# Optimization experiments

Measured on AMD Instinct MI355X. Metric: run time of the kernel, lower is better.

Reference implementation:

```python
import jax, jax.numpy as jnp
import numpy as np
from jax import lax

B, T, H, IN = 1024, 100, 512, 4  # batch, seq len (fixed 100 in source), hidden, nucleotide dim


def _lstm_cell(x, h, c, Wih, Whh, b):
    # PyTorch gate order: i, f, g, o ; b = b_ih + b_hh
    gates = x @ Wih.T + h @ Whh.T + b
    i, f, g, o = jnp.split(gates, 4, axis=-1)
    c = jax.nn.sigmoid(f) * c + jax.nn.sigmoid(i) * jnp.tanh(g)
    h = jax.nn.sigmoid(o) * jnp.tanh(c)
    return h, c


def _run_layer(xs, Wih, Whh, b):
    # xs: [T, B, in] -> ys: [T, B, H], final (h, c)
    Bn = xs.shape[1]
    h0 = jnp.zeros((Bn, H), xs.dtype)
    c0 = jnp.zeros((Bn, H), xs.dtype)

    def step(carry, x):
        h, c = carry
        h, c = _lstm_cell(x, h, c, Wih, Whh, b)
        return (h, c), h

    (h, c), ys = lax.scan(step, (h0, c0), xs)
    return ys, h, c


def setup_inputs() -> dict:
    key = jax.random.key(0)
    ks = jax.random.split(key, 16)
    s = lambda fan: 1.0 / np.sqrt(fan)

    def W(k, shape, fan):
        return jax.random.uniform(k, shape, jnp.float32, -s(fan), s(fan))

    inp = {
        "X": jax.random.normal(ks[0], (B, T, IN), jnp.float32),
        "epoch": 10,
        # encoder LSTM (2 layers)
        "enc_Wih0": W(ks[1], (4 * H, IN), H),
        "enc_Whh0": W(ks[2], (4 * H, H), H),
        "enc_b0": jnp.zeros((4 * H,), jnp.float32),
        "enc_Wih1": W(ks[3], (4 * H, H), H),
        "enc_Whh1": W(ks[4], (4 * H, H), H),
        "enc_b1": jnp.zeros((4 * H,), jnp.float32),
        # decoder LSTM (2 layers, input dim = seq_in_dim = 4)
        "dec_Wih0": W(ks[5], (4 * H, IN), H),
        "dec_Whh0": W(ks[6], (4 * H, H), H),
        "dec_b0": jnp.zeros((4 * H,), jnp.float32),
        "dec_Wih1": W(ks[7], (4 * H, H), H),
        "dec_Whh1": W(ks[8], (4 * H, H), H),
        "dec_b1": jnp.zeros((4 * H,), jnp.float32),
        # predict_MLP = Linear(H, 4)
        "Wp": W(ks[9], (IN, H), H),
        "bp": jnp.zeros((IN,), jnp.float32),
    }
    return inp


def reference(X, epoch, enc_Wih0, enc_Whh0, enc_b0, enc_Wih1, enc_Whh1, enc_b1,
              dec_Wih0, dec_Whh0, dec_b0, dec_Wih1, dec_Whh1, dec_b1, Wp, bp):
    # ---- Encoder: 2-layer LSTM over X (batch_first -> scan over time) ----
    xs = jnp.swapaxes(X, 0, 1)  # [T, B, 4]
    ys0, h0e, c0e = _run_layer(xs, enc_Wih0, enc_Whh0, enc_b0)
    _, h1e, c1e = _run_layer(ys0, enc_Wih1, enc_Whh1, enc_b1)

    #      discretize_input=False) ----
    Bn = X.shape[0]
    x_init = jnp.zeros((Bn, IN), X.dtype)

    def dec_step(carry, _):
        x, h0, c0, h1, c1 = carry
        h0, c0 = _lstm_cell(x, h0, c0, dec_Wih0, dec_Whh0, dec_b0)
        h1, c1 = _lstm_cell(h0, h1, c1, dec_Wih1, dec_Whh1, dec_b1)
        pred = h1 @ Wp.T + bp                 # [B, 4] logits
        x_next = jax.nn.softmax(pred, axis=-1)
        return (x_next, h0, c0, h1, c1), pred

    _, preds = lax.scan(dec_step, (x_init, h0e, c0e, h1e, c1e), None, length=T)
    # out_seq list of [B,1,4] in torch -> stacked [B, 100, 4]
    return jnp.swapaxes(preds, 0, 1)
```

## Files before the change

### kernel.cpp

```cpp
#include <hip/hip_runtime.h>
#include <math.h>
#include <stdint.h>

typedef _Float16 f16;
typedef _Float16 f16x8 __attribute__((ext_vector_type(8)));
typedef float f32x4 __attribute__((ext_vector_type(4)));

#define BATCH 1024
#define HD    512
#define TST   100
#define BUFSZ 49152

__device__ __forceinline__ float4 coh_ld_x4(const void* p) {
    float4 v;
    asm volatile("global_load_dwordx4 %0, %1, off sc0 sc1" : "=v"(v) : "v"(p) : "memory");
    return v;
}
__device__ __forceinline__ float4 ld_x4(const void* p) {
    float4 v;
    asm volatile("global_load_dwordx4 %0, %1, off" : "=v"(v) : "v"(p) : "memory");
    return v;
}
__device__ __forceinline__ void coh_store_u32(uint32_t* p, uint32_t v) {
    asm volatile("global_store_dword %0, %1, off sc0 sc1" :: "v"(p), "v"(v) : "memory");
}
__device__ __forceinline__ void coh_store_i32(int* p, int v) {
    asm volatile("global_store_dword %0, %1, off sc0 sc1" :: "v"(p), "v"(v) : "memory");
}
__device__ __forceinline__ int coh_load_i32(const int* p) {
    int v;
    asm volatile("global_load_dword %0, %1, off sc0 sc1\n\ts_waitcnt vmcnt(0)"
                 : "=v"(v) : "v"(p) : "memory");
    return v;
}
__device__ __forceinline__ void drain_vm() {
    asm volatile("s_waitcnt vmcnt(0)" ::: "memory");
    __builtin_amdgcn_sched_barrier(0);
}

__global__ void split_w(const float* __restrict__ src0, int ksplit,
                        const float* __restrict__ src1, int NKT, f16* __restrict__ out)
{
    int c = blockIdx.x * 256 + threadIdx.x;
    int total = 16 * NKT * 2048;
    if (c >= total) return;
    int u = c & 2047;
    int t2 = c >> 11;
    int kt = t2 % NKT;
    int mt = t2 / NKT;
    int line = u >> 4;
    int s = (u & 15) ^ (line & 15);
    int plane = s >> 3, o = s & 7;
    int m = mt * 128 + line;
    int row = (m & 3) * HD + (m >> 2);
    int kb = kt * 64 + o * 8;
    f16 v[8];
    #pragma unroll
    for (int e = 0; e < 8; ++e) {
        int k = kb + e;
        float w = (k < ksplit) ? src0[(size_t)row * ksplit + k]
                               : src1[(size_t)row * HD + (k - ksplit)];
        float w32 = w * 32.0f;
        f16 hi = (f16)w32;
        v[e] = plane ? (f16)((w32 - (float)hi) * 2048.0f) : hi;
    }
    *(f16x8*)(out + (size_t)c * 8) = *(f16x8*)v;
}

__global__ void prep_b4(const float* __restrict__ b, float* __restrict__ bt) {
    int c = blockIdx.x * 256 + threadIdx.x;
    if (c < 2048) bt[c] = b[(c & 3) * HD + (c >> 2)];
}

__global__ void prep_wih4(const float* __restrict__ W, float* __restrict__ o) {
    int c = blockIdx.x * 256 + threadIdx.x;
    if (c < 8192) {
        int j = c & 3, g = (c >> 2) & 3, hl = c >> 4;
        o[c] = W[(size_t)(g * HD + hl) * 4 + j];
    }
}

__device__ __forceinline__ void publish(int* cell, int epoch) {
    drain_vm();
    __syncthreads();
    if (threadIdx.x == 0)
        coh_store_i32(cell, epoch);
}

__device__ __forceinline__ void wait2(const int* a, int ta, const int* b, int tb) {
    if (threadIdx.x < 64) {
        const int l = threadIdx.x & 15;
        const bool useB = (threadIdx.x & 16) != 0;
        const int* p = (useB ? b : a) + l * 16;
        const int tgt = useB ? tb : ta;
        for (;;) {
            int v = coh_load_i32(p);
            if (__all(v >= tgt)) break;
            __builtin_amdgcn_s_sleep(2);
        }
    }
    __syncthreads();
}

template<int NKT, bool RANK4>
__device__ __forceinline__ void layer_step(
    const f16* __restrict__ Wst, const f16* __restrict__ src1, const f16* __restrict__ src2,
    const float* __restrict__ wih4, const float* __restrict__ xin, int xstride,
    const float* __restrict__ bt4, float* __restrict__ cT, f16* __restrict__ hout,
    char* smem, int mt, int nt)
{
    const int tid = threadIdx.x;
    const int lane = tid & 63;
    const int wv = tid >> 6;
    const int wm = wv & 1, wn = wv >> 1;
    const int l15 = lane & 15, j = lane >> 4;
    const int n0 = nt * 64;

    const int q = (j ^ l15) << 4;
    int ALr[4], BLb[2];
    #pragma unroll
    for (int f = 0; f < 4; ++f) ALr[f] = (wm * 64 + f * 16 + l15) * 256;
    #pragma unroll
    for (int fn = 0; fn < 2; ++fn) BLb[fn] = 32768 + (wn * 32 + fn * 16 + l15) * 256;

    float4 ra[8], rb0[4], rb1[4], xv[2];

    auto issueA = [&](int kt) {
        const f16* ga = Wst + ((size_t)mt * NKT + kt) * 2048 * 8;
        #pragma unroll
        for (int i = 0; i < 8; ++i)
            ra[i] = ld_x4(ga + (size_t)(i * 256 + tid) * 8);
    };
    auto issueB = [&](int kt, float4 (&rb)[4]) {
        #pragma unroll
        for (int i = 0; i < 4; ++i) {
            int v = i * 256 + tid;
            int line = v >> 4;
            int s = (v & 15) ^ (line & 15);
            int ks = kt * 64 + (s & 7) * 8;
            const f16* sp = src1; int kl = ks;
            if (NKT == 16 && ks >= 512) { sp = src2; kl = ks - 512; }
            rb[i] = coh_ld_x4(sp + (size_t)(n0 + line) * 1024 + (s >> 3) * 512 + kl);
        }
    };

    f32x4 accA[4][2] = {};
    f32x4 accB[4][2] = {};

    auto step = [&](int kt, float4 (&rb)[4], bool last) {
        char* buf = smem + (kt & 1) * BUFSZ;
        if (last) asm volatile("s_waitcnt vmcnt(0)" ::: "memory");
        else      asm volatile("s_waitcnt vmcnt(4)" ::: "memory");
        __builtin_amdgcn_sched_barrier(0);
        #pragma unroll
        for (int i = 0; i < 8; ++i) *(float4*)(buf + (i * 256 + tid) * 16) = ra[i];
        #pragma unroll
        for (int i = 0; i < 4; ++i) *(float4*)(buf + 32768 + (i * 256 + tid) * 16) = rb[i];
        if (kt + 1 < NKT) issueA(kt + 1);
        if (kt + 2 < NKT) issueB(kt + 2, rb);
        __syncthreads();
        #pragma unroll
        for (int i = 0; i < 2; ++i) {
            const int off = (i << 6) ^ q;
            f16x8 ah[4], al[4], bh[2], bl[2];
            #pragma unroll
            for (int f = 0; f < 4; ++f) {
                ah[f] = *(const f16x8*)(buf + ALr[f] + off);
                al[f] = *(const f16x8*)(buf + ALr[f] + (off ^ 0x80));
            }
            #pragma unroll
            for (int fn = 0; fn < 2; ++fn) {
                bh[fn] = *(const f16x8*)(buf + BLb[fn] + off);
                bl[fn] = *(const f16x8*)(buf + BLb[fn] + (off ^ 0x80));
            }
            #pragma unroll
            for (int f = 0; f < 4; ++f)
                #pragma unroll
                for (int fn = 0; fn < 2; ++fn) {
                    accA[f][fn] = __builtin_amdgcn_mfma_f32_16x16x32_f16(ah[f], bh[fn], accA[f][fn], 0, 0, 0);
                    accB[f][fn] = __builtin_amdgcn_mfma_f32_16x16x32_f16(al[f], bh[fn], accB[f][fn], 0, 0, 0);
                    accB[f][fn] = __builtin_amdgcn_mfma_f32_16x16x32_f16(ah[f], bl[fn], accB[f][fn], 0, 0, 0);
                }
        }
    };

    if (RANK4) {
        #pragma unroll
        for (int fn = 0; fn < 2; ++fn) {
            const int n = n0 + wn * 32 + fn * 16 + l15;
            xv[fn] = coh_ld_x4(xin + (size_t)n * xstride);
        }
    }
    issueB(0, rb0);
    issueA(0);
    issueB(1, rb1);

    for (int kt = 0; kt < NKT; kt += 2) {
        step(kt,     rb0, false);
        step(kt + 1, rb1, kt + 2 == NKT);
    }

    const float sA = 1.0f / 1024.0f;
    const float sB = 1.0f / (1024.0f * 2048.0f);

    uint32_t* htile = (uint32_t*)smem;
    #pragma unroll
    for (int f = 0; f < 4; ++f) {
        const int hl_loc = wm * 16 + f * 4 + j;
        const int hl = mt * 32 + hl_loc;
        const float4 bv = *(const float4*)(bt4 + hl * 4);
        #pragma unroll
        for (int fn = 0; fn < 2; ++fn) {
            const int n_loc = wn * 32 + fn * 16 + l15;
            const int n = n0 + n_loc;
            float g0 = accA[f][fn][0] * sA + accB[f][fn][0] * sB + bv.x;
            float g1 = accA[f][fn][1] * sA + accB[f][fn][1] * sB + bv.y;
            float g2 = accA[f][fn][2] * sA + accB[f][fn][2] * sB + bv.z;
            float g3 = accA[f][fn][3] * sA + accB[f][fn][3] * sB + bv.w;
            if (RANK4) {
                const float4* wr = (const float4*)(wih4 + hl * 16);
                const float4 x4 = xv[fn];
                g0 += wr[0].x * x4.x + wr[0].y * x4.y + wr[0].z * x4.z + wr[0].w * x4.w;
                g1 += wr[1].x * x4.x + wr[1].y * x4.y + wr[1].z * x4.z + wr[1].w * x4.w;
                g2 += wr[2].x * x4.x + wr[2].y * x4.y + wr[2].z * x4.z + wr[2].w * x4.w;
                g3 += wr[3].x * x4.x + wr[3].y * x4.y + wr[3].z * x4.z + wr[3].w * x4.w;
            }
            const size_t co = (size_t)hl * 1024 + n;
            const float cold = cT[co];
            const float si = 1.0f / (1.0f + expf(-g0));
            const float sf = 1.0f / (1.0f + expf(-g1));
            const float so = 1.0f / (1.0f + expf(-g3));
            const float cn = sf * cold + si * tanhf(g2);
            const float hn = so * tanhf(cn);
            cT[co] = cn;
            const float h32 = hn * 32.0f;
            const f16 hi = (f16)h32;
            const f16 lo = (f16)((h32 - (float)hi) * 2048.0f);
            uint32_t pk = ((uint32_t)__builtin_bit_cast(uint16_t, lo) << 16)
                        | (uint32_t)__builtin_bit_cast(uint16_t, hi);
            htile[n_loc * 33 + hl_loc] = pk;
        }
    }
    __syncthreads();
    uint32_t* h32out = (uint32_t*)hout;
    #pragma unroll
    for (int i = 0; i < 8; ++i) {
        int u = i * 256 + tid;
        int n_loc = u >> 5;
        int r = u & 31;
        int plane = r >> 4;
        int p = r & 15;
        uint32_t t0 = htile[n_loc * 33 + 2 * p];
        uint32_t t1 = htile[n_loc * 33 + 2 * p + 1];
        uint32_t w = plane ? ((t1 & 0xffff0000u) | (t0 >> 16))
                           : ((t1 << 16) | (t0 & 0xffffu));
        coh_store_u32(h32out + (size_t)(n0 + n_loc) * 512 + plane * 256 + mt * 16 + p, w);
    }
}

__device__ __forceinline__ void pred_step(
    const f16* __restrict__ h1, const float* __restrict__ Wp, const float* __restrict__ bp,
    float* __restrict__ outp, float* __restrict__ xfb, int t, int mt, int nt)
{
    const int lane = threadIdx.x & 63;
    const int wv = threadIdx.x >> 6;
    const int n = nt * 64 + mt * 4 + wv;
    const f16* hr = h1 + (size_t)n * 1024;
    const int k0 = lane * 8;
    float4 hv4 = coh_ld_x4(hr + k0);
    float4 lv4 = coh_ld_x4(hr + 512 + k0);
    drain_vm();
    f16x8 hv = __builtin_bit_cast(f16x8, hv4);
    f16x8 lv = __builtin_bit_cast(f16x8, lv4);
    float h[8];
    #pragma unroll
    for (int e = 0; e < 8; ++e)
        h[e] = (float)hv[e] * 0.03125f + (float)lv[e] * (1.0f / 65536.0f);
    float a[4] = {};
    #pragma unroll
    for (int g = 0; g < 4; ++g) {
        const float4 wa = *(const float4*)(Wp + g * HD + k0);
        const float4 wb = *(const float4*)(Wp + g * HD + k0 + 4);
        a[g] = h[0]*wa.x + h[1]*wa.y + h[2]*wa.z + h[3]*wa.w
             + h[4]*wb.x + h[5]*wb.y + h[6]*wb.z + h[7]*wb.w;
    }
    #pragma unroll
    for (int off = 32; off > 0; off >>= 1) {
        a[0] += __shfl_xor(a[0], off);
        a[1] += __shfl_xor(a[1], off);
        a[2] += __shfl_xor(a[2], off);
        a[3] += __shfl_xor(a[3], off);
    }
    if (lane == 0) {
        const float4 bv = *(const float4*)bp;
        float v0 = a[0] + bv.x, v1 = a[1] + bv.y, v2 = a[2] + bv.z, v3 = a[3] + bv.w;
        float* op = outp + (size_t)n * (TST * 4) + t * 4;
        op[0] = v0; op[1] = v1; op[2] = v2; op[3] = v3;
        float m = fmaxf(fmaxf(v0, v1), fmaxf(v2, v3));
        float e0 = expf(v0 - m), e1 = expf(v1 - m), e2 = expf(v2 - m), e3 = expf(v3 - m);
        float inv = 1.0f / (e0 + e1 + e2 + e3);
        uint32_t* xp = (uint32_t*)(xfb + n * 4);
        float s0 = e0 * inv, s1 = e1 * inv, s2 = e2 * inv, s3 = e3 * inv;
        coh_store_u32(xp + 0, __builtin_bit_cast(uint32_t, s0));
        coh_store_u32(xp + 1, __builtin_bit_cast(uint32_t, s1));
        coh_store_u32(xp + 2, __builtin_bit_cast(uint32_t, s2));
        coh_store_u32(xp + 3, __builtin_bit_cast(uint32_t, s3));
    }
}

struct Params {
    const f16 *WE0, *WE1, *WD0, *WD1;
    const float *wih4E, *wih4D, *btE0, *btE1, *btD0, *btD1;
    const float *X, *Wp, *bp;
    f16 *h0a, *h0b, *h1a, *h1b;
    float *c0, *c1;
    float *xfb0, *xfb1;
    float *out;
    int *f0, *f1, *fp;
};

__launch_bounds__(256, 1) __global__ void lstm_persistent(Params P)
{
    __shared__ __align__(16) char smem[2 * BUFSZ];
    const int bx = blockIdx.x;
    const int mt = ((bx & 7) << 1) | ((bx >> 3) & 1);
    const int nt = bx >> 4;
    int* f0g = P.f0 + nt * 256;
    int* f1g = P.f1 + nt * 256;
    int* fpg = P.fp + nt * 256;
    int* my0 = f0g + mt * 16;
    int* my1 = f1g + mt * 16;
    int* myp = fpg + mt * 16;
    f16* h0b_[2] = { P.h0a, P.h0b };
    f16* h1b_[2] = { P.h1a, P.h1b };
    float* xfb_[2] = { P.xfb0, P.xfb1 };

    for (int u = 0; u < 2 * TST; ++u) {
        const bool enc = (u < TST);
        const int t = enc ? u : u - TST;

        if (enc) wait2(f0g, u, f0g, u);
        else     wait2(f0g, u, fpg, t);
        layer_step<8, true>(enc ? P.WE0 : P.WD0,
                            h0b_[(u + 1) & 1], nullptr,
                            enc ? P.wih4E : P.wih4D,
                            enc ? (P.X + t * 4) : xfb_[(t + 1) & 1],
                            enc ? (TST * 4) : 4,
                            enc ? P.btE0 : P.btD0,
                            P.c0, h0b_[u & 1], smem, mt, nt);
        publish(my0, u + 1);

        wait2(f0g, u + 1, f1g, u);
        layer_step<16, false>(enc ? P.WE1 : P.WD1,
                              h0b_[u & 1], h1b_[(u + 1) & 1],
                              nullptr, nullptr, 0,
                              enc ? P.btE1 : P.btD1,
                              P.c1, h1b_[u & 1], smem, mt, nt);
        publish(my1, u + 1);

        if (!enc) {
            wait2(f1g, u + 1, f1g, u + 1);
            pred_step(h1b_[u & 1], P.Wp, P.bp, P.out, xfb_[t & 1], t, mt, nt);
            publish(myp, t + 1);
        }
    }
}

extern "C" void kernel_launch(void* const* d_in, const int* in_sizes, int n_in,
                              void* d_out, int out_size, void* d_ws, size_t ws_size,
                              hipStream_t stream)
{
    const float* X     = (const float*)d_in[0];
    const float* eWih0 = (const float*)d_in[2];
    const float* eWhh0 = (const float*)d_in[3];
    const float* eb0   = (const float*)d_in[4];
    const float* eWih1 = (const float*)d_in[5];
    const float* eWhh1 = (const float*)d_in[6];
    const float* eb1   = (const float*)d_in[7];
    const float* dWih0 = (const float*)d_in[8];
    const float* dWhh0 = (const float*)d_in[9];
    const float* db0   = (const float*)d_in[10];
    const float* dWih1 = (const float*)d_in[11];
    const float* dWhh1 = (const float*)d_in[12];
    const float* db1   = (const float*)d_in[13];
    const float* Wp    = (const float*)d_in[14];
    const float* bp    = (const float*)d_in[15];

    char* ws = (char*)d_ws;
    size_t off = 0;
    auto alloc = [&](size_t bytes) { char* p = ws + off; off += (bytes + 255) & ~(size_t)255; return p; };
    f16* WE0 = (f16*)alloc((size_t)16 * 8  * 2048 * 16);
    f16* WE1 = (f16*)alloc((size_t)16 * 16 * 2048 * 16);
    f16* WD0 = (f16*)alloc((size_t)16 * 8  * 2048 * 16);
    f16* WD1 = (f16*)alloc((size_t)16 * 16 * 2048 * 16);
    float* wih4E = (float*)alloc(8192 * 4);
    float* wih4D = (float*)alloc(8192 * 4);
    float* btE0 = (float*)alloc(2048 * 4);
    float* btE1 = (float*)alloc(2048 * 4);
    float* btD0 = (float*)alloc(2048 * 4);
    float* btD1 = (float*)alloc(2048 * 4);
    f16* h0a = (f16*)alloc((size_t)BATCH * 1024 * 2);
    f16* h0b = (f16*)alloc((size_t)BATCH * 1024 * 2);
    f16* h1a = (f16*)alloc((size_t)BATCH * 1024 * 2);
    f16* h1b = (f16*)alloc((size_t)BATCH * 1024 * 2);
    float* c0  = (float*)alloc((size_t)HD * BATCH * 4);
    float* c1  = (float*)alloc((size_t)HD * BATCH * 4);
    float* xfb0 = (float*)alloc((size_t)BATCH * 4 * 4);
    float* xfb1 = (float*)alloc((size_t)BATCH * 4 * 4);
    int* f0 = (int*)alloc(16 * 256 * 4);
    int* f1 = (int*)alloc(16 * 256 * 4);
    int* fp = (int*)alloc(16 * 256 * 4);
    if (off > ws_size) return;

    split_w<<<(16 * 8  * 2048) / 256, 256, 0, stream>>>(nullptr, 0,   eWhh0, 8,  WE0);
    split_w<<<(16 * 16 * 2048) / 256, 256, 0, stream>>>(eWih1, 512, eWhh1, 16, WE1);
    split_w<<<(16 * 8  * 2048) / 256, 256, 0, stream>>>(nullptr, 0,   dWhh0, 8,  WD0);
    split_w<<<(16 * 16 * 2048) / 256, 256, 0, stream>>>(dWih1, 512, dWhh1, 16, WD1);
    prep_wih4<<<32, 256, 0, stream>>>(eWih0, wih4E);
    prep_wih4<<<32, 256, 0, stream>>>(dWih0, wih4D);
    prep_b4<<<8, 256, 0, stream>>>(eb0, btE0);
    prep_b4<<<8, 256, 0, stream>>>(eb1, btE1);
    prep_b4<<<8, 256, 0, stream>>>(db0, btD0);
    prep_b4<<<8, 256, 0, stream>>>(db1, btD1);

    hipMemsetAsync(h0b, 0, (size_t)BATCH * 1024 * 2, stream);
    hipMemsetAsync(h1b, 0, (size_t)BATCH * 1024 * 2, stream);
    hipMemsetAsync(c0, 0, (size_t)HD * BATCH * 4, stream);
    hipMemsetAsync(c1, 0, (size_t)HD * BATCH * 4, stream);
    hipMemsetAsync(xfb1, 0, (size_t)BATCH * 4 * 4, stream);
    hipMemsetAsync(f0, 0, 16 * 256 * 4, stream);
    hipMemsetAsync(f1, 0, 16 * 256 * 4, stream);
    hipMemsetAsync(fp, 0, 16 * 256 * 4, stream);

    Params P;
    P.WE0 = WE0; P.WE1 = WE1; P.WD0 = WD0; P.WD1 = WD1;
    P.wih4E = wih4E; P.wih4D = wih4D;
    P.btE0 = btE0; P.btE1 = btE1; P.btD0 = btD0; P.btD1 = btD1;
    P.X = X; P.Wp = Wp; P.bp = bp;
    P.h0a = h0a; P.h0b = h0b; P.h1a = h1a; P.h1b = h1b;
    P.c0 = c0; P.c1 = c1;
    P.xfb0 = xfb0; P.xfb1 = xfb1;
    P.out = (float*)d_out;
    P.f0 = f0; P.f1 = f1; P.fp = fp;

    lstm_persistent<<<256, 256, 0, stream>>>(P);

    (void)in_sizes; (void)n_in; (void)out_size;
}
```

Before: 7.493 ms.

## Deepen global-load prefetch pipeline and use fast exp-based activations

Rebuilds the K-loop software pipeline so A tiles are prefetched two stages ahead and B tiles four stages ahead. Register banks rotate and the vmcnt wait thresholds are computed per stage, which hides more global/coherent load latency per recurrent GEMM step. Replaces expf/tanhf in the LSTM cell epilogue with __expf-based sigmoid and a clamped tanh to cut transcendental cost. The deeper prefetch raises VGPR pressure and may lower occupancy, and the fast math slightly changes numerical accuracy.

```diff
diff --git a/kernel.cpp b/kernel.cpp
--- a/kernel.cpp
+++ b/kernel.cpp
@@ -36,6 +36,25 @@
 __device__ __forceinline__ void drain_vm() {
     asm volatile("s_waitcnt vmcnt(0)" ::: "memory");
     __builtin_amdgcn_sched_barrier(0);
+}
+__device__ __forceinline__ void wait_vm(int n) {
+    switch (n) {
+    case 0:  asm volatile("s_waitcnt vmcnt(0)"  ::: "memory"); break;
+    case 8:  asm volatile("s_waitcnt vmcnt(8)"  ::: "memory"); break;
+    case 12: asm volatile("s_waitcnt vmcnt(12)" ::: "memory"); break;
+    case 16: asm volatile("s_waitcnt vmcnt(16)" ::: "memory"); break;
+    default: asm volatile("s_waitcnt vmcnt(20)" ::: "memory"); break;
+    }
+    __builtin_amdgcn_sched_barrier(0);
+}
+
+__device__ __forceinline__ float fast_sig(float x) {
+    return 1.0f / (1.0f + __expf(-x));
+}
+__device__ __forceinline__ float fast_tanh(float x) {
+    float xc = fminf(fmaxf(x, -15.0f), 15.0f);
+    float e = __expf(2.0f * xc);
+    return 1.0f - 2.0f / (e + 1.0f);
 }
 
 __global__ void split_w(const float* __restrict__ src0, int ksplit,
@@ -123,15 +142,17 @@
     #pragma unroll
     for (int fn = 0; fn < 2; ++fn) BLb[fn] = 32768 + (wn * 32 + fn * 16 + l15) * 256;
 
-    float4 ra[8], rb0[4], rb1[4], xv[2];
-
-    auto issueA = [&](int kt) {
+    float4 rak[2][8];
+    float4 rbk[4][4];
+    float4 xv[2];
+
+    auto issueA = [&](int kt, int bank) {
         const f16* ga = Wst + ((size_t)mt * NKT + kt) * 2048 * 8;
         #pragma unroll
         for (int i = 0; i < 8; ++i)
-            ra[i] = ld_x4(ga + (size_t)(i * 256 + tid) * 8);
+            rak[bank][i] = ld_x4(ga + (size_t)(i * 256 + tid) * 8);
     };
-    auto issueB = [&](int kt, float4 (&rb)[4]) {
+    auto issueB = [&](int kt, int bank) {
         #pragma unroll
         for (int i = 0; i < 4; ++i) {
             int v = i * 256 + tid;
@@ -140,24 +161,34 @@
             int ks = kt * 64 + (s & 7) * 8;
             const f16* sp = src1; int kl = ks;
             if (NKT == 16 && ks >= 512) { sp = src2; kl = ks - 512; }
-            rb[i] = coh_ld_x4(sp + (size_t)(n0 + line) * 1024 + (s >> 3) * 512 + kl);
+            rbk[bank][i] = coh_ld_x4(sp + (size_t)(n0 + line) * 1024 + (s >> 3) * 512 + kl);
         }
     };
 
     f32x4 accA[4][2] = {};
     f32x4 accB[4][2] = {};
 
-    auto step = [&](int kt, float4 (&rb)[4], bool last) {
+    if (RANK4) {
+        #pragma unroll
+        for (int fn = 0; fn < 2; ++fn) {
+            const int n = n0 + wn * 32 + fn * 16 + l15;
+            xv[fn] = coh_ld_x4(xin + (size_t)n * xstride);
+        }
+    }
+    issueB(0, 0); issueA(0, 0); issueB(1, 1); issueA(1, 1); issueB(2, 2); issueB(3, 3);
+
+    #pragma unroll
+    for (int kt = 0; kt < NKT; ++kt) {
         char* buf = smem + (kt & 1) * BUFSZ;
-        if (last) asm volatile("s_waitcnt vmcnt(0)" ::: "memory");
-        else      asm volatile("s_waitcnt vmcnt(4)" ::: "memory");
-        __builtin_amdgcn_sched_barrier(0);
-        #pragma unroll
-        for (int i = 0; i < 8; ++i) *(float4*)(buf + (i * 256 + tid) * 16) = ra[i];
-        #pragma unroll
-        for (int i = 0; i < 4; ++i) *(float4*)(buf + 32768 + (i * 256 + tid) * 16) = rb[i];
-        if (kt + 1 < NKT) issueA(kt + 1);
-        if (kt + 2 < NKT) issueB(kt + 2, rb);
+        const int wcnt = (kt == NKT - 1) ? 0 : (kt == NKT - 2) ? 8 :
+                         (kt == NKT - 3) ? 12 : (kt <= 1) ? 20 : 16;
+        wait_vm(wcnt);
+        #pragma unroll
+        for (int i = 0; i < 8; ++i) *(float4*)(buf + (i * 256 + tid) * 16) = rak[kt & 1][i];
+        #pragma unroll
+        for (int i = 0; i < 4; ++i) *(float4*)(buf + 32768 + (i * 256 + tid) * 16) = rbk[kt & 3][i];
+        if (kt + 2 < NKT) issueA(kt + 2, kt & 1);
+        if (kt + 4 < NKT) issueB(kt + 4, kt & 3);
         __syncthreads();
         #pragma unroll
         for (int i = 0; i < 2; ++i) {
@@ -182,22 +213,6 @@
                     accB[f][fn] = __builtin_amdgcn_mfma_f32_16x16x32_f16(ah[f], bl[fn], accB[f][fn], 0, 0, 0);
                 }
         }
-    };
-
-    if (RANK4) {
-        #pragma unroll
-        for (int fn = 0; fn < 2; ++fn) {
-            const int n = n0 + wn * 32 + fn * 16 + l15;
-            xv[fn] = coh_ld_x4(xin + (size_t)n * xstride);
-        }
-    }
-    issueB(0, rb0);
-    issueA(0);
-    issueB(1, rb1);
-
-    for (int kt = 0; kt < NKT; kt += 2) {
-        step(kt,     rb0, false);
-        step(kt + 1, rb1, kt + 2 == NKT);
     }
 
     const float sA = 1.0f / 1024.0f;
@@ -227,11 +242,11 @@
             }
             const size_t co = (size_t)hl * 1024 + n;
             const float cold = cT[co];
-            const float si = 1.0f / (1.0f + expf(-g0));
-            const float sf = 1.0f / (1.0f + expf(-g1));
-            const float so = 1.0f / (1.0f + expf(-g3));
-            const float cn = sf * cold + si * tanhf(g2);
-            const float hn = so * tanhf(cn);
+            const float si = fast_sig(g0);
+            const float sf = fast_sig(g1);
+            const float so = fast_sig(g3);
+            const float cn = sf * cold + si * fast_tanh(g2);
+            const float hn = so * fast_tanh(cn);
             cT[co] = cn;
             const float h32 = hn * 32.0f;
             const f16 hi = (f16)h32;
```

New measurement: 7.382 ms. Within noise of the previous version (-1.5%).
